# Performance work log

Measured on AMD Instinct MI355X. Metric: run time of the kernel, lower is better.

The kernel has to match this reference:

```python
import jax, jax.numpy as jnp
import numpy as np

OUT, IN = 14336, 4096          # Llama FFN up-projection
N = OUT * IN                   # total quantized elements
NB = N // 64                   # NF4 blocks (blocksize 64)
NG = N // 256                  # double-quant groups (group size 256)
B = 32                         # batch rows


def setup_inputs() -> dict:
    key = jax.random.key(0)
    ks = jax.random.split(key, 7)
    x = jax.random.normal(ks[0], (B, IN), dtype=jnp.float16)
    # packed bytes: two 4-bit nibbles per byte (values 0..255)
    packed = jax.random.randint(ks[1], (N // 2,), 0, 256, dtype=jnp.int32)
    absmax = jax.random.uniform(ks[2], (NB,), dtype=jnp.float32)                     # per-block absmax
    code = jax.random.uniform(ks[3], (NB,), jnp.float32, minval=0.5, maxval=1.5)     # per-block code scale
    offset = jax.random.uniform(ks[4], (NB,), jnp.float32, minval=0.0, maxval=8.0)   # per-block offset
    g_absmax = jax.random.uniform(ks[5], (NG,), jnp.float32, minval=0.5, maxval=1.5) # nested (state2) absmax
    g_code = jax.random.uniform(ks[6], (NG,), jnp.float32, minval=0.5, maxval=1.5)   # nested (state2) code
    return {"x": x, "packed": packed, "absmax": absmax, "code": code,
            "offset": offset, "g_absmax": g_absmax, "g_code": g_code}


def _dequantize_nf4(packed, absmax, code, offset, g_absmax, g_code):
    # Unpack nibbles: even element = low nibble (byte & 15), odd = high nibble (byte >> 4)
    low = packed & 15
    high = packed >> 4
    nib = jnp.stack([low, high], axis=-1).reshape(-1).astype(jnp.float32)  # [N]
    # Nested (double) dequantization scales, matching the Triton kernel:
    # combined_scale = (absmax / code) * (g_absmax / g_code)
    block_scale = absmax / code                      # [NB]
    group_scale = g_absmax / g_code                  # [NG]
    cs_block = block_scale * jnp.repeat(group_scale, 64 * 4 // 64)  # each group spans 4 blocks -> [NB]
    cs = jnp.repeat(cs_block, 64)                    # per-element combined scale [N]
    off = jnp.repeat(offset, 64)                     # per-element offset [N]
    # dequantized = nibble * cs - offset * cs (as written in the kernel), stored as fp16
    deq = (nib * cs - off * cs).astype(jnp.float16)
    return deq.reshape(OUT, IN)


def reference(x, packed, absmax, code, offset, g_absmax, g_code):
    W = _dequantize_nf4(packed, absmax, code, offset, g_absmax, g_code)  # [OUT, IN] fp16
    return x @ W.T                                                        # [B, OUT] fp16
```

## Files before the change

### kernel.cpp

```cpp
#include <hip/hip_runtime.h>
#include <hip/hip_bf16.h>


#define OUT_D 14336
#define IN_D  4096
#define B_D   32
#define KC    256
#define OTILE 32
#define NCHUNK (IN_D / KC)
#define LSTRIDE 264

typedef __attribute__((ext_vector_type(4))) float f32x4;
typedef __bf16 bf16x8 __attribute__((ext_vector_type(8)));
typedef __bf16 bf16x4 __attribute__((ext_vector_type(4)));
using u16 = unsigned short;

__global__ __launch_bounds__(256) void nf4_linear_kernel(
    const float* __restrict__ x,
    const int*  __restrict__ packed,
    const float* __restrict__ absmax,
    const float* __restrict__ code,
    const float* __restrict__ offset,
    const float* __restrict__ g_absmax,
    const float* __restrict__ g_code,
    float* __restrict__ out)
{
    __shared__ u16 wlds[OTILE * LSTRIDE];
    __shared__ u16 xlds[B_D * LSTRIDE];

    const int t      = threadIdx.x;
    const int o_base = blockIdx.x * OTILE;

    const int wrow = t >> 3;
    const int wseg = t & 7;
    const int o    = o_base + wrow;

    const int wave   = t >> 6;
    const int lane   = t & 63;
    const int m_base = (wave & 1) * 16;
    const int n_base = (wave >> 1) * 16;
    const int frow   = lane & 15;
    const int kk     = (lane >> 4) * 8;

    f32x4 acc = {0.f, 0.f, 0.f, 0.f};

    for (int kc = 0; kc < NCHUNK; ++kc) {
        #pragma unroll
        for (int j = 0; j < 8; ++j) {
            int li = t + j * 256;
            int xr = li >> 6;
            int xc = (li & 63) * 4;
            f32x4 v = *reinterpret_cast<const f32x4*>(x + xr * IN_D + kc * KC + xc);
            bf16x4 h;
            h[0] = (__bf16)v[0]; h[1] = (__bf16)v[1];
            h[2] = (__bf16)v[2]; h[3] = (__bf16)v[3];
            *reinterpret_cast<bf16x4*>(&xlds[xr * LSTRIDE + xc]) = h;
        }

        const int bidx = o * 64 + kc * 4 + (wseg >> 1);
        const int gidx = o * 16 + kc;
        const float cs  = (absmax[bidx] / code[bidx]) * (g_absmax[gidx] / g_code[gidx]);
        const float noc = -offset[bidx] * cs;

        const int* psrc = packed + o * (IN_D / 2) + kc * (KC / 2) + wseg * 16;
        #pragma unroll
        for (int j = 0; j < 4; ++j) {
            bf16x8 r;
            #pragma unroll
            for (int wi = 0; wi < 4; ++wi) {
                int w = psrc[j * 4 + wi];
                float lo = (float)(w & 15);
                float hi = (float)((w >> 4) & 15);
                r[wi * 2]     = (__bf16)fmaf(lo, cs, noc);
                r[wi * 2 + 1] = (__bf16)fmaf(hi, cs, noc);
            }
            *reinterpret_cast<bf16x8*>(&wlds[wrow * LSTRIDE + wseg * 32 + j * 8]) = r;
        }
        __syncthreads();

        const u16* xrow_p = &xlds[(m_base + frow) * LSTRIDE + kk];
        const u16* wrow_p = &wlds[(n_base + frow) * LSTRIDE + kk];
        #pragma unroll
        for (int ks = 0; ks < KC / 32; ++ks) {
            bf16x8 a = *reinterpret_cast<const bf16x8*>(xrow_p + ks * 32);
            bf16x8 b = *reinterpret_cast<const bf16x8*>(wrow_p + ks * 32);
            acc = __builtin_amdgcn_mfma_f32_16x16x32_bf16(a, b, acc, 0, 0, 0);
        }
        __syncthreads();
    }

    const int oc = o_base + n_base + frow;
    const int r0 = m_base + (lane >> 4) * 4;
    #pragma unroll
    for (int i = 0; i < 4; ++i) {
        out[(r0 + i) * OUT_D + oc] = acc[i];
    }
}

extern "C" void kernel_launch(void* const* d_in, const int* in_sizes, int n_in,
                              void* d_out, int out_size, void* d_ws, size_t ws_size,
                              hipStream_t stream) {
    const void* px = nullptr;
    const void* ppk = nullptr;
    const void* trio[3] = {nullptr, nullptr, nullptr};
    const void* pair[2] = {nullptr, nullptr};
    int ntrio = 0, npair = 0;
    const int SZ_X   = B_D * IN_D;
    const int SZ_PK  = OUT_D * (IN_D / 2);
    const int SZ_NB  = OUT_D * (IN_D / 64);
    const int SZ_NG  = OUT_D * (IN_D / 256);
    for (int i = 0; i < n_in; ++i) {
        int s = in_sizes[i];
        if (s == SZ_X) px = d_in[i];
        else if (s == SZ_PK) ppk = d_in[i];
        else if (s == SZ_NB) { if (ntrio < 3) trio[ntrio++] = d_in[i]; }
        else if (s == SZ_NG) { if (npair < 2) pair[npair++] = d_in[i]; }
    }
    if (!px || !ppk || ntrio != 3 || npair != 2) {
        px = d_in[0]; ppk = d_in[1];
        trio[0] = d_in[2]; trio[1] = d_in[3]; trio[2] = d_in[4];
        pair[0] = d_in[5]; pair[1] = d_in[6];
    }

    nf4_linear_kernel<<<dim3(OUT_D / OTILE), dim3(256), 0, stream>>>(
        (const float*)px, (const int*)ppk,
        (const float*)trio[0], (const float*)trio[1], (const float*)trio[2],
        (const float*)pair[0], (const float*)pair[1],
        (float*)d_out);
}
```

Before: 41.19 us.

## Split K across blocks with atomics, double-buffer weights, read x directly

Splits the K dimension across two blocks per output tile, which doubles the grid to fill more CUs, and combines the partial sums with atomicAdd into an output zeroed by a memset. The weight LDS tile is double-buffered so the second barrier per chunk can be dropped, and the next chunk's packed weights are prefetched into registers with vector loads. The x tile is no longer staged in LDS; each wave reads fp32 x straight from global/cache and converts it to bf16 per MFMA. This adds atomic traffic, a memset launch, and repeated global x reads.

```diff
diff --git a/kernel.cpp b/kernel.cpp
--- a/kernel.cpp
+++ b/kernel.cpp
@@ -7,12 +7,13 @@
 #define B_D   32
 #define KC    256
 #define OTILE 32
-#define NCHUNK (IN_D / KC)
+#define KSPLIT 2
+#define CHUNKS (IN_D / KC / KSPLIT)
 #define LSTRIDE 264
 
 typedef __attribute__((ext_vector_type(4))) float f32x4;
+typedef __attribute__((ext_vector_type(4))) int   i32x4;
 typedef __bf16 bf16x8 __attribute__((ext_vector_type(8)));
-typedef __bf16 bf16x4 __attribute__((ext_vector_type(4)));
 using u16 = unsigned short;
 
 __global__ __launch_bounds__(256) void nf4_linear_kernel(
@@ -25,11 +26,12 @@
     const float* __restrict__ g_code,
     float* __restrict__ out)
 {
-    __shared__ u16 wlds[OTILE * LSTRIDE];
-    __shared__ u16 xlds[B_D * LSTRIDE];
+    __shared__ u16 wlds[2][OTILE * LSTRIDE];
 
     const int t      = threadIdx.x;
     const int o_base = blockIdx.x * OTILE;
+    const int kz     = blockIdx.y;
+    const int kc0    = kz * CHUNKS;
 
     const int wrow = t >> 3;
     const int wseg = t & 7;
@@ -44,56 +46,68 @@
 
     f32x4 acc = {0.f, 0.f, 0.f, 0.f};
 
-    for (int kc = 0; kc < NCHUNK; ++kc) {
+    i32x4 pk[4];
+    {
+        const i32x4* ps = reinterpret_cast<const i32x4*>(
+            packed + o * (IN_D / 2) + kc0 * (KC / 2) + wseg * 16);
         #pragma unroll
-        for (int j = 0; j < 8; ++j) {
-            int li = t + j * 256;
-            int xr = li >> 6;
-            int xc = (li & 63) * 4;
-            f32x4 v = *reinterpret_cast<const f32x4*>(x + xr * IN_D + kc * KC + xc);
-            bf16x4 h;
-            h[0] = (__bf16)v[0]; h[1] = (__bf16)v[1];
-            h[2] = (__bf16)v[2]; h[3] = (__bf16)v[3];
-            *reinterpret_cast<bf16x4*>(&xlds[xr * LSTRIDE + xc]) = h;
-        }
+        for (int j = 0; j < 4; ++j) pk[j] = ps[j];
+    }
+
+    int p = 0;
+    for (int i = 0; i < CHUNKS; ++i) {
+        const int kc = kc0 + i;
 
         const int bidx = o * 64 + kc * 4 + (wseg >> 1);
         const int gidx = o * 16 + kc;
         const float cs  = (absmax[bidx] / code[bidx]) * (g_absmax[gidx] / g_code[gidx]);
         const float noc = -offset[bidx] * cs;
 
-        const int* psrc = packed + o * (IN_D / 2) + kc * (KC / 2) + wseg * 16;
+        u16* wdst = &wlds[p][wrow * LSTRIDE + wseg * 32];
         #pragma unroll
         for (int j = 0; j < 4; ++j) {
             bf16x8 r;
             #pragma unroll
             for (int wi = 0; wi < 4; ++wi) {
-                int w = psrc[j * 4 + wi];
+                int w = pk[j][wi];
                 float lo = (float)(w & 15);
                 float hi = (float)((w >> 4) & 15);
                 r[wi * 2]     = (__bf16)fmaf(lo, cs, noc);
                 r[wi * 2 + 1] = (__bf16)fmaf(hi, cs, noc);
             }
-            *reinterpret_cast<bf16x8*>(&wlds[wrow * LSTRIDE + wseg * 32 + j * 8]) = r;
+            *reinterpret_cast<bf16x8*>(wdst + j * 8) = r;
         }
         __syncthreads();
 
-        const u16* xrow_p = &xlds[(m_base + frow) * LSTRIDE + kk];
-        const u16* wrow_p = &wlds[(n_base + frow) * LSTRIDE + kk];
+        if (i + 1 < CHUNKS) {
+            const i32x4* ps = reinterpret_cast<const i32x4*>(
+                packed + o * (IN_D / 2) + (kc + 1) * (KC / 2) + wseg * 16);
+            #pragma unroll
+            for (int j = 0; j < 4; ++j) pk[j] = ps[j];
+        }
+
+        const float* xbase = x + (m_base + frow) * IN_D + kc * KC + kk;
+        const u16*   wp    = &wlds[p][(n_base + frow) * LSTRIDE + kk];
         #pragma unroll
         for (int ks = 0; ks < KC / 32; ++ks) {
-            bf16x8 a = *reinterpret_cast<const bf16x8*>(xrow_p + ks * 32);
-            bf16x8 b = *reinterpret_cast<const bf16x8*>(wrow_p + ks * 32);
+            f32x4 xa = *reinterpret_cast<const f32x4*>(xbase + ks * 32);
+            f32x4 xb = *reinterpret_cast<const f32x4*>(xbase + ks * 32 + 4);
+            bf16x8 a;
+            a[0] = (__bf16)xa[0]; a[1] = (__bf16)xa[1];
+            a[2] = (__bf16)xa[2]; a[3] = (__bf16)xa[3];
+            a[4] = (__bf16)xb[0]; a[5] = (__bf16)xb[1];
+            a[6] = (__bf16)xb[2]; a[7] = (__bf16)xb[3];
+            bf16x8 b = *reinterpret_cast<const bf16x8*>(wp + ks * 32);
             acc = __builtin_amdgcn_mfma_f32_16x16x32_bf16(a, b, acc, 0, 0, 0);
         }
-        __syncthreads();
+        p ^= 1;
     }
 
     const int oc = o_base + n_base + frow;
     const int r0 = m_base + (lane >> 4) * 4;
     #pragma unroll
     for (int i = 0; i < 4; ++i) {
-        out[(r0 + i) * OUT_D + oc] = acc[i];
+        atomicAdd(&out[(r0 + i) * OUT_D + oc], acc[i]);
     }
 }
 
@@ -122,7 +136,9 @@
         pair[0] = d_in[5]; pair[1] = d_in[6];
     }
 
-    nf4_linear_kernel<<<dim3(OUT_D / OTILE), dim3(256), 0, stream>>>(
+    hipMemsetAsync(d_out, 0, (size_t)out_size * sizeof(float), stream);
+
+    nf4_linear_kernel<<<dim3(OUT_D / OTILE, KSPLIT), dim3(256), 0, stream>>>(
         (const float*)px, (const int*)ppk,
         (const float*)trio[0], (const float*)trio[1], (const float*)trio[2],
         (const float*)pair[0], (const float*)pair[1],
```

Result: slower. 85.55 us (+107.7%).

## Double-buffer LDS and register-prefetch next chunk's weights, x and scales

Applied to the files above, without the earlier changes.

Restructures the K loop so the packed weights, x tile and scale factors for the next chunk are loaded into registers before the current chunk is dequantized and multiplied. LDS tiles are double-buffered, so one barrier per chunk is enough instead of two. Packed weights are now read as 128-bit vector loads instead of scalar int loads. This hides global-load latency behind dequant and MFMA work, at the cost of more registers and twice the LDS, which can lower occupancy.

```diff
diff --git a/kernel.cpp b/kernel.cpp
--- a/kernel.cpp
+++ b/kernel.cpp
@@ -7,10 +7,11 @@
 #define B_D   32
 #define KC    256
 #define OTILE 32
-#define NCHUNK (IN_D / KC)
+#define CHUNKS (IN_D / KC)
 #define LSTRIDE 264
 
 typedef __attribute__((ext_vector_type(4))) float f32x4;
+typedef __attribute__((ext_vector_type(4))) int   i32x4;
 typedef __bf16 bf16x8 __attribute__((ext_vector_type(8)));
 typedef __bf16 bf16x4 __attribute__((ext_vector_type(4)));
 using u16 = unsigned short;
@@ -25,8 +26,8 @@
     const float* __restrict__ g_code,
     float* __restrict__ out)
 {
-    __shared__ u16 wlds[OTILE * LSTRIDE];
-    __shared__ u16 xlds[B_D * LSTRIDE];
+    __shared__ u16 wlds[2][OTILE * LSTRIDE];
+    __shared__ u16 xlds[2][B_D * LSTRIDE];
 
     const int t      = threadIdx.x;
     const int o_base = blockIdx.x * OTILE;
@@ -42,51 +43,91 @@
     const int frow   = lane & 15;
     const int kk     = (lane >> 4) * 8;
 
+    const int* pbase = packed + o * (IN_D / 2) + wseg * 16;
+
     f32x4 acc = {0.f, 0.f, 0.f, 0.f};
 
-    for (int kc = 0; kc < NCHUNK; ++kc) {
-        #pragma unroll
-        for (int j = 0; j < 8; ++j) {
-            int li = t + j * 256;
-            int xr = li >> 6;
-            int xc = (li & 63) * 4;
-            f32x4 v = *reinterpret_cast<const f32x4*>(x + xr * IN_D + kc * KC + xc);
-            bf16x4 h;
-            h[0] = (__bf16)v[0]; h[1] = (__bf16)v[1];
-            h[2] = (__bf16)v[2]; h[3] = (__bf16)v[3];
-            *reinterpret_cast<bf16x4*>(&xlds[xr * LSTRIDE + xc]) = h;
-        }
+    i32x4 pkA[4], pkB[4];
+    f32x4 pxA[8], pxB[8];
+    float amA, cdA, ofA, gaA, gcA;
+    float amB, cdB, ofB, gaB, gcB;
 
-        const int bidx = o * 64 + kc * 4 + (wseg >> 1);
-        const int gidx = o * 16 + kc;
-        const float cs  = (absmax[bidx] / code[bidx]) * (g_absmax[gidx] / g_code[gidx]);
-        const float noc = -offset[bidx] * cs;
+#define LOADPK(DST, KCI) { \
+    const i32x4* ps = reinterpret_cast<const i32x4*>(pbase + (KCI) * (KC / 2)); \
+    DST[0] = ps[0]; DST[1] = ps[1]; DST[2] = ps[2]; DST[3] = ps[3]; }
 
-        const int* psrc = packed + o * (IN_D / 2) + kc * (KC / 2) + wseg * 16;
-        #pragma unroll
-        for (int j = 0; j < 4; ++j) {
-            bf16x8 r;
-            #pragma unroll
-            for (int wi = 0; wi < 4; ++wi) {
-                int w = psrc[j * 4 + wi];
-                float lo = (float)(w & 15);
-                float hi = (float)((w >> 4) & 15);
-                r[wi * 2]     = (__bf16)fmaf(lo, cs, noc);
-                r[wi * 2 + 1] = (__bf16)fmaf(hi, cs, noc);
-            }
-            *reinterpret_cast<bf16x8*>(&wlds[wrow * LSTRIDE + wseg * 32 + j * 8]) = r;
-        }
-        __syncthreads();
+#define LOADPX(DST, KCI) { \
+    const float* xb = x + (KCI) * KC; \
+    _Pragma("unroll") \
+    for (int j = 0; j < 8; ++j) { \
+        int li = t + j * 256; \
+        DST[j] = *reinterpret_cast<const f32x4*>(xb + (li >> 6) * IN_D + (li & 63) * 4); } }
 
-        const u16* xrow_p = &xlds[(m_base + frow) * LSTRIDE + kk];
-        const u16* wrow_p = &wlds[(n_base + frow) * LSTRIDE + kk];
-        #pragma unroll
-        for (int ks = 0; ks < KC / 32; ++ks) {
-            bf16x8 a = *reinterpret_cast<const bf16x8*>(xrow_p + ks * 32);
-            bf16x8 b = *reinterpret_cast<const bf16x8*>(wrow_p + ks * 32);
-            acc = __builtin_amdgcn_mfma_f32_16x16x32_bf16(a, b, acc, 0, 0, 0);
-        }
-        __syncthreads();
+#define LOADSC(AM, CD, OF, GA, GC, KCI) { \
+    int bidx = o * 64 + (KCI) * 4 + (wseg >> 1); \
+    int gidx = o * 16 + (KCI); \
+    AM = absmax[bidx]; CD = code[bidx]; OF = offset[bidx]; \
+    GA = g_absmax[gidx]; GC = g_code[gidx]; }
+
+#define BODY(PK, PX, AM, CD, OF, GA, GC, PKN, PXN, AMN, CDN, OFN, GAN, GCN, KCI) { \
+     \
+    if ((KCI) + 1 < CHUNKS) { \
+        LOADPK(PKN, (KCI) + 1); \
+        LOADPX(PXN, (KCI) + 1); \
+        LOADSC(AMN, CDN, OFN, GAN, GCN, (KCI) + 1); \
+    } \
+     \
+    { \
+        const float cs  = (AM / CD) * (GA / GC); \
+        const float noc = -OF * cs; \
+        u16* wdst = &wlds[p][wrow * LSTRIDE + wseg * 32]; \
+        _Pragma("unroll") \
+        for (int j = 0; j < 4; ++j) { \
+            bf16x8 r; \
+            _Pragma("unroll") \
+            for (int wi = 0; wi < 4; ++wi) { \
+                int w = PK[j][wi]; \
+                r[wi * 2]     = (__bf16)fmaf((float)(w & 15),        cs, noc); \
+                r[wi * 2 + 1] = (__bf16)fmaf((float)((w >> 4) & 15), cs, noc); \
+            } \
+            *reinterpret_cast<bf16x8*>(wdst + j * 8) = r; \
+        } \
+    } \
+     \
+    { \
+        _Pragma("unroll") \
+        for (int j = 0; j < 8; ++j) { \
+            int li = t + j * 256; \
+            bf16x4 h; \
+            h[0] = (__bf16)PX[j][0]; h[1] = (__bf16)PX[j][1]; \
+            h[2] = (__bf16)PX[j][2]; h[3] = (__bf16)PX[j][3]; \
+            *reinterpret_cast<bf16x4*>(&xlds[p][(li >> 6) * LSTRIDE + (li & 63) * 4]) = h; \
+        } \
+    } \
+    __syncthreads(); \
+     \
+    { \
+        const u16* xp = &xlds[p][(m_base + frow) * LSTRIDE + kk]; \
+        const u16* wp = &wlds[p][(n_base + frow) * LSTRIDE + kk]; \
+        _Pragma("unroll") \
+        for (int ks = 0; ks < KC / 32; ++ks) { \
+            bf16x8 a = *reinterpret_cast<const bf16x8*>(xp + ks * 32); \
+            bf16x8 b = *reinterpret_cast<const bf16x8*>(wp + ks * 32); \
+            acc = __builtin_amdgcn_mfma_f32_16x16x32_bf16(a, b, acc, 0, 0, 0); \
+        } \
+    } \
+    p ^= 1; }
+
+    LOADPK(pkA, 0);
+    LOADPX(pxA, 0);
+    LOADSC(amA, cdA, ofA, gaA, gcA, 0);
+
+    int p = 0;
+    for (int ic = 0; ic < CHUNKS; ic += 2) {
+        BODY(pkA, pxA, amA, cdA, ofA, gaA, gcA,
+             pkB, pxB, amB, cdB, ofB, gaB, gcB, ic);
+        BODY(pkB, pxB, amB, cdB, ofB, gaB, gcB,
+             pkA, pxA, amA, cdA, ofA, gaA, gcA, ic + 1);
     }
 
     const int oc = o_base + n_base + frow;
```

Result: slower. 42.31 us (+2.7%).
